# Kernel optimization log

Hardware: AMD Instinct MI355X
Metric: run time of the kernel (lower is better)

The kernel has to match this reference:

```python
import jax, jax.numpy as jnp
import numpy as np

PAD_WORD = 1  # index of PAD in tgt_dict


def setup_inputs() -> dict:
    key = jax.random.key(0)
    k1, k2, k3, k4, k5 = jax.random.split(key, 5)
    N, D, S = 1024, 1024, 64   # N = tlen*batch rows, D = input_size, S = slen
    B, V = 64, 32000           # batch, vocab
    hidden = jax.random.normal(k1, (N, D), dtype=jnp.float32)
    attn = jax.random.uniform(k2, (N, S), dtype=jnp.float32)
    src = jax.random.randint(k3, (S, B, 1), 0, V)
    W = jax.random.normal(k4, (V, D), dtype=jnp.float32) * 0.02
    w_copy = jax.random.normal(k5, (D, 1), dtype=jnp.float32) * 0.02
    b_copy = jnp.zeros((1,), dtype=jnp.float32)
    return {"hidden": hidden, "attn": attn, "src": src, "W": W,
            "w_copy": w_copy, "b_copy": b_copy}


def reference(hidden, attn, src, W, w_copy, b_copy):
    V = W.shape[0]
    B = src.shape[1]
    T = hidden.shape[0] // B  # tlen
    # copy gate: sigmoid(Linear(hidden, 1))  -> [N, 1]
    p_copy = jax.nn.sigmoid(hidden @ w_copy + b_copy)
    # tied-embedding projection -> [N, V], pad column masked to -inf
    logits = hidden @ W.T
    logits = logits.at[:, PAD_WORD].set(-jnp.inf)
    prob = jax.nn.softmax(logits, axis=1) + 1e-20
    # gated generation prob, reshaped to [T, B*V]
    prob = ((1.0 - p_copy) * prob).reshape(T, B * V)
    # flattened source indices with per-batch vocab offsets -> [B*S]
    batch_offset = (jnp.arange(B) * V)[:, None]
    idx = (src[:, :, 0].T + batch_offset).reshape(-1)
    # gated copy attention, reshaped to [T, B*S]
    attn_w = (p_copy * attn).reshape(T, -1)
    # scatter-add copy mass into the vocab distribution (duplicates accumulate)
    out = prob.at[:, idx].add(attn_w)
    return out.reshape(T * B, V)
```

## Files before the change

kernel.cpp:

```cpp
#include <hip/hip_runtime.h>
#include <stdint.h>

typedef unsigned short u16;
typedef unsigned int u32;

#define NROWS 1024
#define DDIM  1024
#define SLEN  64
#define BATCH 64
#define VOCAB 32000
#define NBN2  125
#define PAD_WORD 1

typedef __attribute__((ext_vector_type(4))) float f32x4;
typedef __attribute__((ext_vector_type(8))) short s16x8;

__device__ __forceinline__ u16 f2bf(float x) {
  union { float f; u32 u; } v; v.f = x;
  u32 r = v.u + 0x7FFF + ((v.u >> 16) & 1);
  return (u16)(r >> 16);
}
__device__ __forceinline__ float bf2f(u16 x) {
  union { u32 u; float f; } v; v.u = ((u32)x) << 16;
  return v.f;
}

__global__ __launch_bounds__(256) void prep_convw_kernel(
    const float* __restrict__ hidden, const float* __restrict__ w_copy,
    const float* __restrict__ b_copy, u16* __restrict__ hbf,
    float* __restrict__ pcopy, const float* __restrict__ W,
    u16* __restrict__ Wb)
{
  const int tid = threadIdx.x;
  if (blockIdx.x < NROWS) {
    const int n = blockIdx.x;
    float4 h = ((const float4*)(hidden + (size_t)n * DDIM))[tid];
    float4 w = ((const float4*)w_copy)[tid];
    ushort4 hb;
    hb.x = f2bf(h.x); hb.y = f2bf(h.y); hb.z = f2bf(h.z); hb.w = f2bf(h.w);
    ((ushort4*)(hbf + (size_t)n * DDIM))[tid] = hb;
    float d = h.x * w.x + h.y * w.y + h.z * w.z + h.w * w.w;
    #pragma unroll
    for (int m = 1; m < 64; m <<= 1) d += __shfl_xor(d, m);
    __shared__ float ws4[4];
    if ((tid & 63) == 0) ws4[tid >> 6] = d;
    __syncthreads();
    if (tid == 0) {
      float s = ws4[0] + ws4[1] + ws4[2] + ws4[3] + b_copy[0];
      pcopy[n] = 1.0f / (1.0f + __expf(-s));
    }
    return;
  }
  const int total = VOCAB * DDIM / 8;
  const int stride = (gridDim.x - NROWS) * 256;
  for (int i = (blockIdx.x - NROWS) * 256 + tid; i < total; i += stride) {
    const float4* p = (const float4*)(W + (size_t)i * 8);
    float4 a = p[0], b = p[1];
    uint4 q;
    q.x = (u32)f2bf(a.x) | ((u32)f2bf(a.y) << 16);
    q.y = (u32)f2bf(a.z) | ((u32)f2bf(a.w) << 16);
    q.z = (u32)f2bf(b.x) | ((u32)f2bf(b.y) << 16);
    q.w = (u32)f2bf(b.z) | ((u32)f2bf(b.w) << 16);
    *((uint4*)(Wb + (size_t)i * 8)) = q;
  }
}

__global__ __launch_bounds__(512, 2) void gemm_exp_kernel(
    const u16* __restrict__ A, const u16* __restrict__ B,
    float* __restrict__ out, u16* __restrict__ ebf,
    float* __restrict__ partial, const int use_bf16)
{
  __shared__ u16 lA[2][16384];
  __shared__ u16 lB[2][16384];
  __shared__ float rowacc[4][256];

  const int tid  = threadIdx.x;
  const int lane = tid & 63;
  const int wid  = tid >> 6;
  const int wm   = wid >> 2;
  const int wn   = wid & 3;
  const int al   = lane & 15;
  const int ks   = lane >> 4;

  const int orig = blockIdx.x;
  const int xcd  = orig & 7;
  const int idx  = orig >> 3;
  const int wg   = (xcd < 4 ? xcd * 63 : 252 + (xcd - 4) * 62) + idx;
  const int bm   = wg & 3;
  const int bn   = wg >> 2;

  const u16* Abase = A + (size_t)(bm * 256) * DDIM;
  const u16* Bbase = B + (size_t)(bn * 256) * DDIM;

  const int s0  = wid * 128 + lane;
  const int rr0 = s0 >> 3;
  const int cs0 = (s0 & 7) ^ (rr0 & 7);

#define STAGE(gptr, lptr) do { \
    __builtin_amdgcn_global_load_lds( \
        (const __attribute__((address_space(1))) u32*)((gptr) + (size_t)rr0 * DDIM + cs0 * 8), \
        (__attribute__((address_space(3))) u32*)((lptr) + s0 * 8), 16, 0, 0); \
    __builtin_amdgcn_global_load_lds( \
        (const __attribute__((address_space(1))) u32*)((gptr) + (size_t)(rr0 + 8) * DDIM + cs0 * 8), \
        (__attribute__((address_space(3))) u32*)((lptr) + s0 * 8 + 512), 16, 0, 0); \
  } while (0)

#define WL(n) do { asm volatile("s_waitcnt lgkmcnt(" #n ")" ::: "memory"); \
                   __builtin_amdgcn_sched_barrier(0); } while (0)
#define WV(n) do { asm volatile("s_waitcnt vmcnt(" #n ")" ::: "memory"); \
                   __builtin_amdgcn_sched_barrier(0); } while (0)
#define BAR() do { __builtin_amdgcn_sched_barrier(0); \
                   __builtin_amdgcn_s_barrier(); \
                   __builtin_amdgcn_sched_barrier(0); } while (0)

#define RD_ALO(buf) do { \
    _Pragma("unroll") \
    for (int mi = 0; mi < 4; ++mi) { \
      const u16* p_ = (buf) + wm * 8192 + (mi * 16 + al) * 64; \
      alo[mi][0] = *(const s16x8*)(p_ + (ks ^ (al & 7)) * 8); \
      alo[mi][1] = *(const s16x8*)(p_ + ((4 + ks) ^ (al & 7)) * 8); \
    } } while (0)
#define RD_AHI(buf) do { \
    _Pragma("unroll") \
    for (int mi = 0; mi < 4; ++mi) { \
      const u16* p_ = (buf) + wm * 8192 + (64 + mi * 16 + al) * 64; \
      ahi[mi][0] = *(const s16x8*)(p_ + (ks ^ (al & 7)) * 8); \
      ahi[mi][1] = *(const s16x8*)(p_ + ((4 + ks) ^ (al & 7)) * 8); \
    } } while (0)
#define RD_B0(buf) do { \
    _Pragma("unroll") \
    for (int ni = 0; ni < 2; ++ni) { \
      const u16* p_ = (buf) + (wn >> 1) * 8192 + ((wn & 1) * 64 + ni * 16 + al) * 64; \
      b0f[ni][0] = *(const s16x8*)(p_ + (ks ^ (al & 7)) * 8); \
      b0f[ni][1] = *(const s16x8*)(p_ + ((4 + ks) ^ (al & 7)) * 8); \
    } } while (0)
#define RD_B1(buf) do { \
    _Pragma("unroll") \
    for (int ni = 0; ni < 2; ++ni) { \
      const u16* p_ = (buf) + (wn >> 1) * 8192 + ((wn & 1) * 64 + 32 + ni * 16 + al) * 64; \
      b1f[ni][0] = *(const s16x8*)(p_ + (ks ^ (al & 7)) * 8); \
      b1f[ni][1] = *(const s16x8*)(p_ + ((4 + ks) ^ (al & 7)) * 8); \
    } } while (0)
#define MM(AF, BF, r0, c0) do { \
    __builtin_amdgcn_s_setprio(1); \
    _Pragma("unroll") \
    for (int mi = 0; mi < 4; ++mi) \
      _Pragma("unroll") \
      for (int ni = 0; ni < 2; ++ni) \
        _Pragma("unroll") \
        for (int kk = 0; kk < 2; ++kk) \
          acc[(r0) + mi][(c0) + ni] = __builtin_amdgcn_mfma_f32_16x16x32_bf16( \
              AF[mi][kk], BF[ni][kk], acc[(r0) + mi][(c0) + ni], 0, 0, 0); \
    __builtin_amdgcn_s_setprio(0); \
  } while (0)

  u16* lAc = &lA[0][0]; u16* lBc = &lB[0][0];
  u16* lAn = &lA[1][0]; u16* lBn = &lB[1][0];

  STAGE(Abase,              lAc);
  STAGE(Abase + 128 * DDIM, lAc + 8192);
  STAGE(Bbase,              lBc);
  STAGE(Bbase + 128 * DDIM, lBc + 8192);
  STAGE(Abase + 64,         lAn);
  WV(2);
  BAR();

  f32x4 acc[8][4];
  #pragma unroll
  for (int i = 0; i < 8; ++i)
    #pragma unroll
    for (int j = 0; j < 4; ++j)
      acc[i][j] = (f32x4){0.f, 0.f, 0.f, 0.f};

  s16x8 alo[4][2], ahi[4][2], b0f[2][2], b1f[2][2];

  RD_ALO(lAc); RD_B0(lBc); RD_B1(lBc);
  STAGE(Abase + 128 * DDIM + 64, lAn + 8192);

  for (int t = 0; t < 15; ++t) {
    const int kt1 = (t + 1) * 64;
    const int kt2 = (t + 2) * 64;
    WL(4);
    MM(alo, b0f, 0, 0);
    STAGE(Bbase + kt1, lBn);
    RD_AHI(lAc);
    WL(8);
    MM(alo, b1f, 0, 2);
    STAGE(Bbase + 128 * DDIM + kt1, lBn + 8192);
    WL(0);
    MM(ahi, b0f, 4, 0);
    BAR();
    if (t < 14) STAGE(Abase + kt2, lAc);
    WV(2);
    BAR();
    RD_ALO(lAn); RD_B0(lBn);
    MM(ahi, b1f, 4, 2);
    RD_B1(lBn);
    if (t < 14) STAGE(Abase + 128 * DDIM + kt2, lAc + 8192);
    u16* tp = lAc; lAc = lAn; lAn = tp;
    tp = lBc; lBc = lBn; lBn = tp;
  }
  WL(4);
  MM(alo, b0f, 0, 0);
  RD_AHI(lAc);
  WL(8);
  MM(alo, b1f, 0, 2);
  WL(0);
  MM(ahi, b0f, 4, 0);
  MM(ahi, b1f, 4, 2);

#undef STAGE
#undef WL
#undef WV
#undef BAR

  const int g = ks;
  float rsum[8][4];
  #pragma unroll
  for (int mi = 0; mi < 8; ++mi)
    #pragma unroll
    for (int j = 0; j < 4; ++j) rsum[mi][j] = 0.f;

  const size_t grow0 = (size_t)(bm * 256 + wm * 128);
  const int gcol0 = bn * 256 + wn * 64;
  #pragma unroll
  for (int mi = 0; mi < 8; ++mi) {
    const int rofs = (mi >> 2) * 64 + (mi & 3) * 16 + g * 4;
    #pragma unroll
    for (int j = 0; j < 4; ++j) {
      const size_t row = grow0 + rofs + j;
      #pragma unroll
      for (int ni = 0; ni < 4; ++ni) {
        const int col = gcol0 + (ni >> 1) * 32 + (ni & 1) * 16 + al;
        float e = __expf(acc[mi][ni >> 1][(ni & 1) * 2 + 0] * 0.f +
                         0.f);
        (void)e;
      }
    }
  }
  #pragma unroll
  for (int mi = 0; mi < 8; ++mi) {
    const int rofs = (mi >> 2) * 64 + (mi & 3) * 16 + g * 4;
    #pragma unroll
    for (int j = 0; j < 4; ++j) {
      const size_t row = grow0 + rofs + j;
      #pragma unroll
      for (int ni = 0; ni < 4; ++ni) {
        const int col = gcol0 + (ni >> 1) * 32 + (ni & 1) * 16 + al;
        float e = __expf(acc[mi][ni][j]);
        if (col == PAD_WORD) e = 0.f;
        rsum[mi][j] += e;
        if (use_bf16) ebf[row * VOCAB + col] = f2bf(e);
        else          out[row * VOCAB + col] = e;
      }
    }
  }
  #pragma unroll
  for (int mi = 0; mi < 8; ++mi)
    #pragma unroll
    for (int j = 0; j < 4; ++j) {
      float v = rsum[mi][j];
      v += __shfl_xor(v, 1);
      v += __shfl_xor(v, 2);
      v += __shfl_xor(v, 4);
      v += __shfl_xor(v, 8);
      rsum[mi][j] = v;
    }
  if (al == 0) {
    #pragma unroll
    for (int mi = 0; mi < 8; ++mi)
      #pragma unroll
      for (int j = 0; j < 4; ++j)
        rowacc[wn][wm * 128 + (mi >> 2) * 64 + (mi & 3) * 16 + g * 4 + j] =
            rsum[mi][j];
  }
  __syncthreads();
  if (tid < 256)
    partial[(size_t)bn * NROWS + bm * 256 + tid] =
        rowacc[0][tid] + rowacc[1][tid] + rowacc[2][tid] + rowacc[3][tid];
}

__global__ __launch_bounds__(256) void rowsum_kernel(
    const float* __restrict__ partial, const float* __restrict__ pcopy,
    float* __restrict__ scale, float* __restrict__ ofs)
{
  const int n = blockIdx.x * 256 + threadIdx.x;
  if (n >= NROWS) return;
  float s = 0.f;
  for (int j = 0; j < NBN2; ++j) s += partial[(size_t)j * NROWS + n];
  const float p = pcopy[n];
  scale[n] = (1.0f - p) / s;
  ofs[n]   = (1.0f - p) * 1e-20f;
}

__global__ __launch_bounds__(256) void norm_bf16_kernel(
    const u16* __restrict__ ebf, float* __restrict__ out,
    const float* __restrict__ scale, const float* __restrict__ ofs)
{
  const int total8 = NROWS * VOCAB / 8;
  const int stride = gridDim.x * blockDim.x;
  for (int i = blockIdx.x * 256 + threadIdx.x; i < total8; i += stride) {
    const int n = i / (VOCAB / 8);
    ushort4 v0 = ((const ushort4*)ebf)[i * 2];
    ushort4 v1 = ((const ushort4*)ebf)[i * 2 + 1];
    const float sc = scale[n], of = ofs[n];
    float4 o0, o1;
    o0.x = bf2f(v0.x) * sc + of; o0.y = bf2f(v0.y) * sc + of;
    o0.z = bf2f(v0.z) * sc + of; o0.w = bf2f(v0.w) * sc + of;
    o1.x = bf2f(v1.x) * sc + of; o1.y = bf2f(v1.y) * sc + of;
    o1.z = bf2f(v1.z) * sc + of; o1.w = bf2f(v1.w) * sc + of;
    ((float4*)out)[i * 2]     = o0;
    ((float4*)out)[i * 2 + 1] = o1;
  }
}

__global__ __launch_bounds__(256) void norm_kernel(
    float* __restrict__ out, const float* __restrict__ scale,
    const float* __restrict__ ofs)
{
  const int total4 = NROWS * VOCAB / 4;
  const int stride = gridDim.x * blockDim.x;
  for (int i = blockIdx.x * 256 + threadIdx.x; i < total4; i += stride) {
    const int n = i / (VOCAB / 4);
    float4* p = (float4*)out + i;
    float4 v = *p;
    const float sc = scale[n], of = ofs[n];
    v.x = v.x * sc + of;
    v.y = v.y * sc + of;
    v.z = v.z * sc + of;
    v.w = v.w * sc + of;
    *p = v;
  }
}

__global__ __launch_bounds__(256) void scatter_kernel(
    float* __restrict__ out, const float* __restrict__ attn,
    const int* __restrict__ src, const float* __restrict__ pcopy)
{
  const int t = blockIdx.x * 256 + threadIdx.x;
  const int n = t >> 6;
  const int s = t & 63;
  const int b = n & (BATCH - 1);
  const int v = src[s * BATCH + b];
  const float w = pcopy[n] * attn[(size_t)n * SLEN + s];
  atomicAdd(out + (size_t)n * VOCAB + v, w);
}

extern "C" void kernel_launch(void* const* d_in, const int* in_sizes, int n_in,
                              void* d_out, int out_size, void* d_ws, size_t ws_size,
                              hipStream_t stream) {
  const float* hidden = (const float*)d_in[0];
  const float* attn   = (const float*)d_in[1];
  const int*   src    = (const int*)d_in[2];
  const float* W      = (const float*)d_in[3];
  const float* w_copy = (const float*)d_in[4];
  const float* b_copy = (const float*)d_in[5];
  float* out = (float*)d_out;

  char* ws = (char*)d_ws;
  u16*   Wb      = (u16*)ws;
  u16*   hbf     = (u16*)(ws + 65536000);
  float* pcopy   = (float*)(ws + 67633152);
  float* partial = (float*)(ws + 67637248);
  float* scale   = (float*)(ws + 68661248);
  float* ofs     = (float*)(ws + 68665344);
  u16*   ebf     = (u16*)(ws + 68669440);
  const size_t need_bf16 = 68669440ull + 65536000ull;
  const int use_bf16 = (ws_size >= need_bf16) ? 1 : 0;

  prep_convw_kernel<<<NROWS + 2048, 256, 0, stream>>>(
      hidden, w_copy, b_copy, hbf, pcopy, W, Wb);
  gemm_exp_kernel<<<4 * NBN2, 512, 0, stream>>>(hbf, Wb, out, ebf, partial, use_bf16);
  rowsum_kernel<<<(NROWS + 255) / 256, 256, 0, stream>>>(partial, pcopy, scale, ofs);
  if (use_bf16)
    norm_bf16_kernel<<<2048, 256, 0, stream>>>(ebf, out, scale, ofs);
  else
    norm_kernel<<<2048, 256, 0, stream>>>(out, scale, ofs);
  scatter_kernel<<<NROWS * SLEN / 256, 256, 0, stream>>>(out, attn, src, pcopy);
}
```

Baseline: 165.0 us.

## Fuse W fp32-to-bf16 conversion into GEMM B-tile staging

Drops the separate pass that converted the whole 32000x1024 W matrix to bf16 in the workspace. The GEMM now loads fp32 W rows into registers, converts them with a round-half-up pack, and writes swizzled bf16 into LDS, while A keeps its direct global-to-LDS path. The main loop is rescheduled around register prefetch of the next B tile. This removes a 128MB read plus 64MB write, but each W tile is now read as fp32 by all four M-blocks, which doubles B traffic inside the GEMM and adds conversion ALU work and waits to the main loop. Rounding changes slightly (no ties-to-even) and a dead exp loop is removed.

```diff
diff --git a/kernel.cpp b/kernel.cpp
--- a/kernel.cpp
+++ b/kernel.cpp
@@ -24,49 +24,37 @@
   union { u32 u; float f; } v; v.u = ((u32)x) << 16;
   return v.f;
 }
-
-__global__ __launch_bounds__(256) void prep_convw_kernel(
+__device__ __forceinline__ u32 pkbf(float a, float b) {
+  union { float f; u32 u; } va, vb; va.f = a; vb.f = b;
+  return ((va.u + 0x8000u) >> 16) | ((vb.u + 0x8000u) & 0xFFFF0000u);
+}
+
+__global__ __launch_bounds__(256) void prep_kernel(
     const float* __restrict__ hidden, const float* __restrict__ w_copy,
     const float* __restrict__ b_copy, u16* __restrict__ hbf,
-    float* __restrict__ pcopy, const float* __restrict__ W,
-    u16* __restrict__ Wb)
-{
+    float* __restrict__ pcopy)
+{
+  const int n = blockIdx.x;
   const int tid = threadIdx.x;
-  if (blockIdx.x < NROWS) {
-    const int n = blockIdx.x;
-    float4 h = ((const float4*)(hidden + (size_t)n * DDIM))[tid];
-    float4 w = ((const float4*)w_copy)[tid];
-    ushort4 hb;
-    hb.x = f2bf(h.x); hb.y = f2bf(h.y); hb.z = f2bf(h.z); hb.w = f2bf(h.w);
-    ((ushort4*)(hbf + (size_t)n * DDIM))[tid] = hb;
-    float d = h.x * w.x + h.y * w.y + h.z * w.z + h.w * w.w;
-    #pragma unroll
-    for (int m = 1; m < 64; m <<= 1) d += __shfl_xor(d, m);
-    __shared__ float ws4[4];
-    if ((tid & 63) == 0) ws4[tid >> 6] = d;
-    __syncthreads();
-    if (tid == 0) {
-      float s = ws4[0] + ws4[1] + ws4[2] + ws4[3] + b_copy[0];
-      pcopy[n] = 1.0f / (1.0f + __expf(-s));
-    }
-    return;
-  }
-  const int total = VOCAB * DDIM / 8;
-  const int stride = (gridDim.x - NROWS) * 256;
-  for (int i = (blockIdx.x - NROWS) * 256 + tid; i < total; i += stride) {
-    const float4* p = (const float4*)(W + (size_t)i * 8);
-    float4 a = p[0], b = p[1];
-    uint4 q;
-    q.x = (u32)f2bf(a.x) | ((u32)f2bf(a.y) << 16);
-    q.y = (u32)f2bf(a.z) | ((u32)f2bf(a.w) << 16);
-    q.z = (u32)f2bf(b.x) | ((u32)f2bf(b.y) << 16);
-    q.w = (u32)f2bf(b.z) | ((u32)f2bf(b.w) << 16);
-    *((uint4*)(Wb + (size_t)i * 8)) = q;
+  float4 h = ((const float4*)(hidden + (size_t)n * DDIM))[tid];
+  float4 w = ((const float4*)w_copy)[tid];
+  ushort4 hb;
+  hb.x = f2bf(h.x); hb.y = f2bf(h.y); hb.z = f2bf(h.z); hb.w = f2bf(h.w);
+  ((ushort4*)(hbf + (size_t)n * DDIM))[tid] = hb;
+  float d = h.x * w.x + h.y * w.y + h.z * w.z + h.w * w.w;
+  #pragma unroll
+  for (int m = 1; m < 64; m <<= 1) d += __shfl_xor(d, m);
+  __shared__ float ws4[4];
+  if ((tid & 63) == 0) ws4[tid >> 6] = d;
+  __syncthreads();
+  if (tid == 0) {
+    float s = ws4[0] + ws4[1] + ws4[2] + ws4[3] + b_copy[0];
+    pcopy[n] = 1.0f / (1.0f + __expf(-s));
   }
 }
 
 __global__ __launch_bounds__(512, 2) void gemm_exp_kernel(
-    const u16* __restrict__ A, const u16* __restrict__ B,
+    const u16* __restrict__ A, const float* __restrict__ Wf,
     float* __restrict__ out, u16* __restrict__ ebf,
     float* __restrict__ partial, const int use_bf16)
 {
@@ -90,19 +78,55 @@
   const int bn   = wg >> 2;
 
   const u16* Abase = A + (size_t)(bm * 256) * DDIM;
-  const u16* Bbase = B + (size_t)(bn * 256) * DDIM;
 
   const int s0  = wid * 128 + lane;
   const int rr0 = s0 >> 3;
   const int cs0 = (s0 & 7) ^ (rr0 & 7);
 
-#define STAGE(gptr, lptr) do { \
+#define STAGEH(gptr, lptr) do { \
     __builtin_amdgcn_global_load_lds( \
         (const __attribute__((address_space(1))) u32*)((gptr) + (size_t)rr0 * DDIM + cs0 * 8), \
         (__attribute__((address_space(3))) u32*)((lptr) + s0 * 8), 16, 0, 0); \
     __builtin_amdgcn_global_load_lds( \
         (const __attribute__((address_space(1))) u32*)((gptr) + (size_t)(rr0 + 8) * DDIM + cs0 * 8), \
         (__attribute__((address_space(3))) u32*)((lptr) + s0 * 8 + 512), 16, 0, 0); \
+  } while (0)
+#define STAGE_A(lptr, kt) do { \
+    STAGEH(Abase + (kt), (lptr)); \
+    STAGEH(Abase + 128 * DDIM + (kt), (lptr) + 8192); \
+  } while (0)
+
+  const int brow_st = tid >> 2;
+  const int bk0     = (tid & 3) * 16;
+  const float* Bsrc0 = Wf + (size_t)(bn * 256 + brow_st) * DDIM + bk0;
+  const float* Bsrc1 = Bsrc0 + (size_t)128 * DDIM;
+  f32x4 br[8];
+
+#define ISSUE_B(kt) do { \
+    br[0] = *(const f32x4*)(Bsrc0 + (kt));      \
+    br[1] = *(const f32x4*)(Bsrc0 + (kt) + 4);  \
+    br[2] = *(const f32x4*)(Bsrc0 + (kt) + 8);  \
+    br[3] = *(const f32x4*)(Bsrc0 + (kt) + 12); \
+    br[4] = *(const f32x4*)(Bsrc1 + (kt));      \
+    br[5] = *(const f32x4*)(Bsrc1 + (kt) + 4);  \
+    br[6] = *(const f32x4*)(Bsrc1 + (kt) + 8);  \
+    br[7] = *(const f32x4*)(Bsrc1 + (kt) + 12); \
+  } while (0)
+
+  union pk8 { u32 w[4]; s16x8 v; };
+#define CVT_WRITE_B(dstbase) do { \
+    _Pragma("unroll") \
+    for (int h_ = 0; h_ < 2; ++h_) { \
+      _Pragma("unroll") \
+      for (int j_ = 0; j_ < 2; ++j_) { \
+        pk8 p_; \
+        f32x4 f0_ = br[h_ * 4 + j_ * 2], f1_ = br[h_ * 4 + j_ * 2 + 1]; \
+        p_.w[0] = pkbf(f0_.x, f0_.y); p_.w[1] = pkbf(f0_.z, f0_.w); \
+        p_.w[2] = pkbf(f1_.x, f1_.y); p_.w[3] = pkbf(f1_.z, f1_.w); \
+        const int sl_ = (((tid & 3) * 2 + j_) ^ (brow_st & 7)); \
+        *(s16x8*)((dstbase) + h_ * 8192 + brow_st * 64 + sl_ * 8) = p_.v; \
+      } \
+    } \
   } while (0)
 
 #define WL(n) do { asm volatile("s_waitcnt lgkmcnt(" #n ")" ::: "memory"); \
@@ -157,12 +181,13 @@
   u16* lAc = &lA[0][0]; u16* lBc = &lB[0][0];
   u16* lAn = &lA[1][0]; u16* lBn = &lB[1][0];
 
-  STAGE(Abase,              lAc);
-  STAGE(Abase + 128 * DDIM, lAc + 8192);
-  STAGE(Bbase,              lBc);
-  STAGE(Bbase + 128 * DDIM, lBc + 8192);
-  STAGE(Abase + 64,         lAn);
-  WV(2);
+  ISSUE_B(0);
+  STAGE_A(lAc, 0);
+  WV(4);
+  CVT_WRITE_B(lBc);
+  ISSUE_B(64);
+  WV(8);
+  WL(0);
   BAR();
 
   f32x4 acc[8][4];
@@ -174,32 +199,26 @@
 
   s16x8 alo[4][2], ahi[4][2], b0f[2][2], b1f[2][2];
 
-  RD_ALO(lAc); RD_B0(lBc); RD_B1(lBc);
-  STAGE(Abase + 128 * DDIM + 64, lAn + 8192);
-
   for (int t = 0; t < 15; ++t) {
-    const int kt1 = (t + 1) * 64;
-    const int kt2 = (t + 2) * 64;
+    RD_ALO(lAc); RD_B0(lBc); RD_B1(lBc);
+    WV(0);
+    CVT_WRITE_B(lBn);
+    STAGE_A(lAn, (t + 1) * 64);
+    if (t < 14) ISSUE_B((t + 2) * 64);
+    WL(8);
+    MM(alo, b0f, 0, 0);
     WL(4);
-    MM(alo, b0f, 0, 0);
-    STAGE(Bbase + kt1, lBn);
+    MM(alo, b1f, 0, 2);
     RD_AHI(lAc);
-    WL(8);
-    MM(alo, b1f, 0, 2);
-    STAGE(Bbase + 128 * DDIM + kt1, lBn + 8192);
     WL(0);
     MM(ahi, b0f, 4, 0);
+    if (t < 14) { WV(8); } else { WV(0); }
     BAR();
-    if (t < 14) STAGE(Abase + kt2, lAc);
-    WV(2);
-    BAR();
-    RD_ALO(lAn); RD_B0(lBn);
     MM(ahi, b1f, 4, 2);
-    RD_B1(lBn);
-    if (t < 14) STAGE(Abase + 128 * DDIM + kt2, lAc + 8192);
     u16* tp = lAc; lAc = lAn; lAn = tp;
     tp = lBc; lBc = lBn; lBn = tp;
   }
+  RD_ALO(lAc); RD_B0(lBc); RD_B1(lBc);
   WL(4);
   MM(alo, b0f, 0, 0);
   RD_AHI(lAc);
@@ -209,7 +228,10 @@
   MM(ahi, b0f, 4, 0);
   MM(ahi, b1f, 4, 2);
 
-#undef STAGE
+#undef STAGEH
+#undef STAGE_A
+#undef ISSUE_B
+#undef CVT_WRITE_B
 #undef WL
 #undef WV
 #undef BAR
@@ -223,21 +245,6 @@
 
   const size_t grow0 = (size_t)(bm * 256 + wm * 128);
   const int gcol0 = bn * 256 + wn * 64;
-  #pragma unroll
-  for (int mi = 0; mi < 8; ++mi) {
-    const int rofs = (mi >> 2) * 64 + (mi & 3) * 16 + g * 4;
-    #pragma unroll
-    for (int j = 0; j < 4; ++j) {
-      const size_t row = grow0 + rofs + j;
-      #pragma unroll
-      for (int ni = 0; ni < 4; ++ni) {
-        const int col = gcol0 + (ni >> 1) * 32 + (ni & 1) * 16 + al;
-        float e = __expf(acc[mi][ni >> 1][(ni & 1) * 2 + 0] * 0.f +
-                         0.f);
-        (void)e;
-      }
-    }
-  }
   #pragma unroll
   for (int mi = 0; mi < 8; ++mi) {
     const int rofs = (mi >> 2) * 64 + (mi & 3) * 16 + g * 4;
@@ -358,19 +365,17 @@
   float* out = (float*)d_out;
 
   char* ws = (char*)d_ws;
-  u16*   Wb      = (u16*)ws;
-  u16*   hbf     = (u16*)(ws + 65536000);
-  float* pcopy   = (float*)(ws + 67633152);
-  float* partial = (float*)(ws + 67637248);
-  float* scale   = (float*)(ws + 68661248);
-  float* ofs     = (float*)(ws + 68665344);
-  u16*   ebf     = (u16*)(ws + 68669440);
-  const size_t need_bf16 = 68669440ull + 65536000ull;
+  u16*   hbf     = (u16*)ws;
+  float* pcopy   = (float*)(ws + 2097152);
+  float* partial = (float*)(ws + 2101248);
+  float* scale   = (float*)(ws + 3125248);
+  float* ofs     = (float*)(ws + 3129344);
+  u16*   ebf     = (u16*)(ws + 3133440);
+  const size_t need_bf16 = 3133440ull + 65536000ull;
   const int use_bf16 = (ws_size >= need_bf16) ? 1 : 0;
 
-  prep_convw_kernel<<<NROWS + 2048, 256, 0, stream>>>(
-      hidden, w_copy, b_copy, hbf, pcopy, W, Wb);
-  gemm_exp_kernel<<<4 * NBN2, 512, 0, stream>>>(hbf, Wb, out, ebf, partial, use_bf16);
+  prep_kernel<<<NROWS, 256, 0, stream>>>(hidden, w_copy, b_copy, hbf, pcopy);
+  gemm_exp_kernel<<<4 * NBN2, 512, 0, stream>>>(hbf, W, out, ebf, partial, use_bf16);
   rowsum_kernel<<<(NROWS + 255) / 256, 256, 0, stream>>>(partial, pcopy, scale, ofs);
   if (use_bf16)
     norm_bf16_kernel<<<2048, 256, 0, stream>>>(ebf, out, scale, ofs);
```

New measurement: 156.3 us. -5.3%, faster.

## Switch GEMM operands from bf16 to fp8 e4m3 with fp8 MFMA

Applied to the files above, without the earlier changes.

Hidden states and the tied embedding weight are now quantized to fp8 e4m3 instead of bf16, and the GEMM runs on the fp8 16x16x32 MFMA with LDS tiles, staging and swizzle rebuilt for byte elements. The aim is to halve operand bytes in the weight conversion output and GEMM loads and to raise MFMA throughput. The prep kernel is split into a hidden/gate kernel and a separate weight conversion kernel, and a dead exp loop in the epilogue is removed. The cost is much lower precision in the logits, with no per-tensor scaling, which risks accuracy against the fp32 reference.

```diff
diff --git a/kernel.cpp b/kernel.cpp
--- a/kernel.cpp
+++ b/kernel.cpp
@@ -1,6 +1,7 @@
 #include <hip/hip_runtime.h>
 #include <stdint.h>
 
+typedef unsigned char  u8;
 typedef unsigned short u16;
 typedef unsigned int u32;
 
@@ -13,7 +14,6 @@
 #define PAD_WORD 1
 
 typedef __attribute__((ext_vector_type(4))) float f32x4;
-typedef __attribute__((ext_vector_type(8))) short s16x8;
 
 __device__ __forceinline__ u16 f2bf(float x) {
   union { float f; u32 u; } v; v.f = x;
@@ -24,54 +24,68 @@
   union { u32 u; float f; } v; v.u = ((u32)x) << 16;
   return v.f;
 }
-
-__global__ __launch_bounds__(256) void prep_convw_kernel(
+__device__ __forceinline__ u32 f2e4m3(float x) {
+  union { float f; u32 u; } v; v.f = x;
+  const u32 s = (v.u >> 31) << 7;
+  const u32 m = v.u & 0x7FFFFFFFu;
+  if (m < 0x3C800000u) {
+    union { u32 u; float f; } a; a.u = m;
+    int q = (int)rintf(a.f * 512.0f);
+    return s | (u32)q;
+  }
+  u32 u2 = m + 0x7FFFFu + ((m >> 20) & 1);
+  u32 code = (((u2 >> 23) - 120u) << 3) | ((u2 >> 20) & 7u);
+  if (code > 0x7Eu) code = 0x7Eu;
+  return s | code;
+}
+
+__global__ __launch_bounds__(256) void prep_kernel(
     const float* __restrict__ hidden, const float* __restrict__ w_copy,
-    const float* __restrict__ b_copy, u16* __restrict__ hbf,
-    float* __restrict__ pcopy, const float* __restrict__ W,
-    u16* __restrict__ Wb)
-{
+    const float* __restrict__ b_copy, u8* __restrict__ hq,
+    float* __restrict__ pcopy)
+{
+  const int n = blockIdx.x;
   const int tid = threadIdx.x;
-  if (blockIdx.x < NROWS) {
-    const int n = blockIdx.x;
-    float4 h = ((const float4*)(hidden + (size_t)n * DDIM))[tid];
-    float4 w = ((const float4*)w_copy)[tid];
-    ushort4 hb;
-    hb.x = f2bf(h.x); hb.y = f2bf(h.y); hb.z = f2bf(h.z); hb.w = f2bf(h.w);
-    ((ushort4*)(hbf + (size_t)n * DDIM))[tid] = hb;
-    float d = h.x * w.x + h.y * w.y + h.z * w.z + h.w * w.w;
-    #pragma unroll
-    for (int m = 1; m < 64; m <<= 1) d += __shfl_xor(d, m);
-    __shared__ float ws4[4];
-    if ((tid & 63) == 0) ws4[tid >> 6] = d;
-    __syncthreads();
-    if (tid == 0) {
-      float s = ws4[0] + ws4[1] + ws4[2] + ws4[3] + b_copy[0];
-      pcopy[n] = 1.0f / (1.0f + __expf(-s));
-    }
-    return;
-  }
-  const int total = VOCAB * DDIM / 8;
-  const int stride = (gridDim.x - NROWS) * 256;
-  for (int i = (blockIdx.x - NROWS) * 256 + tid; i < total; i += stride) {
-    const float4* p = (const float4*)(W + (size_t)i * 8);
-    float4 a = p[0], b = p[1];
+  float4 h = ((const float4*)(hidden + (size_t)n * DDIM))[tid];
+  float4 w = ((const float4*)w_copy)[tid];
+  u32 q = f2e4m3(h.x) | (f2e4m3(h.y) << 8) | (f2e4m3(h.z) << 16) | (f2e4m3(h.w) << 24);
+  ((u32*)(hq + (size_t)n * DDIM))[tid] = q;
+  float d = h.x * w.x + h.y * w.y + h.z * w.z + h.w * w.w;
+  #pragma unroll
+  for (int m = 1; m < 64; m <<= 1) d += __shfl_xor(d, m);
+  __shared__ float ws4[4];
+  if ((tid & 63) == 0) ws4[tid >> 6] = d;
+  __syncthreads();
+  if (tid == 0) {
+    float s = ws4[0] + ws4[1] + ws4[2] + ws4[3] + b_copy[0];
+    pcopy[n] = 1.0f / (1.0f + __expf(-s));
+  }
+}
+
+__global__ __launch_bounds__(256) void convw8_kernel(
+    const float* __restrict__ W, u8* __restrict__ Wq)
+{
+  const int total = VOCAB * DDIM / 16;
+  const int stride = gridDim.x * blockDim.x;
+  for (int i = blockIdx.x * 256 + threadIdx.x; i < total; i += stride) {
+    const f32x4* p = (const f32x4*)(W + (size_t)i * 16);
+    f32x4 a = p[0], b = p[1], c = p[2], d = p[3];
     uint4 q;
-    q.x = (u32)f2bf(a.x) | ((u32)f2bf(a.y) << 16);
-    q.y = (u32)f2bf(a.z) | ((u32)f2bf(a.w) << 16);
-    q.z = (u32)f2bf(b.x) | ((u32)f2bf(b.y) << 16);
-    q.w = (u32)f2bf(b.z) | ((u32)f2bf(b.w) << 16);
-    *((uint4*)(Wb + (size_t)i * 8)) = q;
+    q.x = f2e4m3(a.x) | (f2e4m3(a.y) << 8) | (f2e4m3(a.z) << 16) | (f2e4m3(a.w) << 24);
+    q.y = f2e4m3(b.x) | (f2e4m3(b.y) << 8) | (f2e4m3(b.z) << 16) | (f2e4m3(b.w) << 24);
+    q.z = f2e4m3(c.x) | (f2e4m3(c.y) << 8) | (f2e4m3(c.z) << 16) | (f2e4m3(c.w) << 24);
+    q.w = f2e4m3(d.x) | (f2e4m3(d.y) << 8) | (f2e4m3(d.z) << 16) | (f2e4m3(d.w) << 24);
+    ((uint4*)Wq)[i] = q;
   }
 }
 
 __global__ __launch_bounds__(512, 2) void gemm_exp_kernel(
-    const u16* __restrict__ A, const u16* __restrict__ B,
+    const u8* __restrict__ A, const u8* __restrict__ B,
     float* __restrict__ out, u16* __restrict__ ebf,
     float* __restrict__ partial, const int use_bf16)
 {
-  __shared__ u16 lA[2][16384];
-  __shared__ u16 lB[2][16384];
+  __shared__ u8 lA[2][16384];
+  __shared__ u8 lB[2][16384];
   __shared__ float rowacc[4][256];
 
   const int tid  = threadIdx.x;
@@ -89,20 +103,19 @@
   const int bm   = wg & 3;
   const int bn   = wg >> 2;
 
-  const u16* Abase = A + (size_t)(bm * 256) * DDIM;
-  const u16* Bbase = B + (size_t)(bn * 256) * DDIM;
-
-  const int s0  = wid * 128 + lane;
-  const int rr0 = s0 >> 3;
-  const int cs0 = (s0 & 7) ^ (rr0 & 7);
-
-#define STAGE(gptr, lptr) do { \
-    __builtin_amdgcn_global_load_lds( \
-        (const __attribute__((address_space(1))) u32*)((gptr) + (size_t)rr0 * DDIM + cs0 * 8), \
-        (__attribute__((address_space(3))) u32*)((lptr) + s0 * 8), 16, 0, 0); \
-    __builtin_amdgcn_global_load_lds( \
-        (const __attribute__((address_space(1))) u32*)((gptr) + (size_t)(rr0 + 8) * DDIM + cs0 * 8), \
-        (__attribute__((address_space(3))) u32*)((lptr) + s0 * 8 + 512), 16, 0, 0); \
+  const u8* Abase = A + (size_t)(bm * 256) * DDIM;
+  const u8* Bbase = B + (size_t)(bn * 256) * DDIM;
+
+  const int sA = wid * 64 + lane;
+  const int rA = sA >> 2;
+  const int cA = (lane & 3) ^ (rA & 3);
+
+#define GLL(gp, lp) __builtin_amdgcn_global_load_lds( \
+    (const __attribute__((address_space(1))) u32*)(gp), \
+    (__attribute__((address_space(3))) u32*)(lp), 16, 0, 0)
+#define STAGE_T(gbase, lptr, kt) do { \
+    GLL((gbase) + (size_t)rA * DDIM + (kt) + cA * 16, (lptr) + sA * 16); \
+    GLL((gbase) + (size_t)(rA + 128) * DDIM + (kt) + cA * 16, (lptr) + 8192 + sA * 16); \
   } while (0)
 
 #define WL(n) do { asm volatile("s_waitcnt lgkmcnt(" #n ")" ::: "memory"); \
@@ -116,30 +129,34 @@
 #define RD_ALO(buf) do { \
     _Pragma("unroll") \
     for (int mi = 0; mi < 4; ++mi) { \
-      const u16* p_ = (buf) + wm * 8192 + (mi * 16 + al) * 64; \
-      alo[mi][0] = *(const s16x8*)(p_ + (ks ^ (al & 7)) * 8); \
-      alo[mi][1] = *(const s16x8*)(p_ + ((4 + ks) ^ (al & 7)) * 8); \
+      const int r_ = wm * 128 + mi * 16 + al; \
+      const u8* p_ = (buf) + r_ * 64 + (ks & 1) * 8; \
+      alo[mi][0] = *(const long*)(p_ + ((((ks >> 1))     ^ (r_ & 3)) * 16)); \
+      alo[mi][1] = *(const long*)(p_ + ((((ks >> 1) + 2) ^ (r_ & 3)) * 16)); \
     } } while (0)
 #define RD_AHI(buf) do { \
     _Pragma("unroll") \
     for (int mi = 0; mi < 4; ++mi) { \
-      const u16* p_ = (buf) + wm * 8192 + (64 + mi * 16 + al) * 64; \
-      ahi[mi][0] = *(const s16x8*)(p_ + (ks ^ (al & 7)) * 8); \
-      ahi[mi][1] = *(const s16x8*)(p_ + ((4 + ks) ^ (al & 7)) * 8); \
+      const int r_ = wm * 128 + 64 + mi * 16 + al; \
+      const u8* p_ = (buf) + r_ * 64 + (ks & 1) * 8; \
+      ahi[mi][0] = *(const long*)(p_ + ((((ks >> 1))     ^ (r_ & 3)) * 16)); \
+      ahi[mi][1] = *(const long*)(p_ + ((((ks >> 1) + 2) ^ (r_ & 3)) * 16)); \
     } } while (0)
 #define RD_B0(buf) do { \
     _Pragma("unroll") \
     for (int ni = 0; ni < 2; ++ni) { \
-      const u16* p_ = (buf) + (wn >> 1) * 8192 + ((wn & 1) * 64 + ni * 16 + al) * 64; \
-      b0f[ni][0] = *(const s16x8*)(p_ + (ks ^ (al & 7)) * 8); \
-      b0f[ni][1] = *(const s16x8*)(p_ + ((4 + ks) ^ (al & 7)) * 8); \
+      const int r_ = wn * 64 + ni * 16 + al; \
+      const u8* p_ = (buf) + r_ * 64 + (ks & 1) * 8; \
+      b0f[ni][0] = *(const long*)(p_ + ((((ks >> 1))     ^ (r_ & 3)) * 16)); \
+      b0f[ni][1] = *(const long*)(p_ + ((((ks >> 1) + 2) ^ (r_ & 3)) * 16)); \
     } } while (0)
 #define RD_B1(buf) do { \
     _Pragma("unroll") \
     for (int ni = 0; ni < 2; ++ni) { \
-      const u16* p_ = (buf) + (wn >> 1) * 8192 + ((wn & 1) * 64 + 32 + ni * 16 + al) * 64; \
-      b1f[ni][0] = *(const s16x8*)(p_ + (ks ^ (al & 7)) * 8); \
-      b1f[ni][1] = *(const s16x8*)(p_ + ((4 + ks) ^ (al & 7)) * 8); \
+      const int r_ = wn * 64 + 32 + ni * 16 + al; \
+      const u8* p_ = (buf) + r_ * 64 + (ks & 1) * 8; \
+      b1f[ni][0] = *(const long*)(p_ + ((((ks >> 1))     ^ (r_ & 3)) * 16)); \
+      b1f[ni][1] = *(const long*)(p_ + ((((ks >> 1) + 2) ^ (r_ & 3)) * 16)); \
     } } while (0)
 #define MM(AF, BF, r0, c0) do { \
     __builtin_amdgcn_s_setprio(1); \
@@ -149,55 +166,49 @@
       for (int ni = 0; ni < 2; ++ni) \
         _Pragma("unroll") \
         for (int kk = 0; kk < 2; ++kk) \
-          acc[(r0) + mi][(c0) + ni] = __builtin_amdgcn_mfma_f32_16x16x32_bf16( \
+          acc[(r0) + mi][(c0) + ni] = __builtin_amdgcn_mfma_f32_16x16x32_fp8_fp8( \
               AF[mi][kk], BF[ni][kk], acc[(r0) + mi][(c0) + ni], 0, 0, 0); \
     __builtin_amdgcn_s_setprio(0); \
   } while (0)
 
-  u16* lAc = &lA[0][0]; u16* lBc = &lB[0][0];
-  u16* lAn = &lA[1][0]; u16* lBn = &lB[1][0];
-
-  STAGE(Abase,              lAc);
-  STAGE(Abase + 128 * DDIM, lAc + 8192);
-  STAGE(Bbase,              lBc);
-  STAGE(Bbase + 128 * DDIM, lBc + 8192);
-  STAGE(Abase + 64,         lAn);
+  u8* lAc = &lA[0][0]; u8* lBc = &lB[0][0];
+  u8* lAn = &lA[1][0]; u8* lBn = &lB[1][0];
+
+  f32x4 acc[8][4];
+  #pragma unroll
+  for (int i = 0; i < 8; ++i)
+    #pragma unroll
+    for (int j = 0; j < 4; ++j)
+      acc[i][j] = (f32x4){0.f, 0.f, 0.f, 0.f};
+
+  long alo[4][2], ahi[4][2], b0f[2][2], b1f[2][2];
+
+  STAGE_T(Abase, lAc, 0);
+  STAGE_T(Bbase, lBc, 0);
+  STAGE_T(Abase, lAn, 64);
   WV(2);
   BAR();
-
-  f32x4 acc[8][4];
-  #pragma unroll
-  for (int i = 0; i < 8; ++i)
-    #pragma unroll
-    for (int j = 0; j < 4; ++j)
-      acc[i][j] = (f32x4){0.f, 0.f, 0.f, 0.f};
-
-  s16x8 alo[4][2], ahi[4][2], b0f[2][2], b1f[2][2];
-
   RD_ALO(lAc); RD_B0(lBc); RD_B1(lBc);
-  STAGE(Abase + 128 * DDIM + 64, lAn + 8192);
 
   for (int t = 0; t < 15; ++t) {
     const int kt1 = (t + 1) * 64;
     const int kt2 = (t + 2) * 64;
     WL(4);
     MM(alo, b0f, 0, 0);
-    STAGE(Bbase + kt1, lBn);
+    STAGE_T(Bbase, lBn, kt1);
     RD_AHI(lAc);
     WL(8);
     MM(alo, b1f, 0, 2);
-    STAGE(Bbase + 128 * DDIM + kt1, lBn + 8192);
     WL(0);
     MM(ahi, b0f, 4, 0);
     BAR();
-    if (t < 14) STAGE(Abase + kt2, lAc);
-    WV(2);
+    if (t < 14) STAGE_T(Abase, lAc, kt2);
+    if (t < 14) { WV(2); } else { WV(0); }
     BAR();
     RD_ALO(lAn); RD_B0(lBn);
     MM(ahi, b1f, 4, 2);
     RD_B1(lBn);
-    if (t < 14) STAGE(Abase + 128 * DDIM + kt2, lAc + 8192);
-    u16* tp = lAc; lAc = lAn; lAn = tp;
+    u8* tp = lAc; lAc = lAn; lAn = tp;
     tp = lBc; lBc = lBn; lBn = tp;
   }
   WL(4);
@@ -209,7 +220,8 @@
   MM(ahi, b0f, 4, 0);
   MM(ahi, b1f, 4, 2);
 
-#undef STAGE
+#undef GLL
+#undef STAGE_T
 #undef WL
 #undef WV
 #undef BAR
@@ -223,21 +235,6 @@
 
   const size_t grow0 = (size_t)(bm * 256 + wm * 128);
   const int gcol0 = bn * 256 + wn * 64;
-  #pragma unroll
-  for (int mi = 0; mi < 8; ++mi) {
-    const int rofs = (mi >> 2) * 64 + (mi & 3) * 16 + g * 4;
-    #pragma unroll
-    for (int j = 0; j < 4; ++j) {
-      const size_t row = grow0 + rofs + j;
-      #pragma unroll
-      for (int ni = 0; ni < 4; ++ni) {
-        const int col = gcol0 + (ni >> 1) * 32 + (ni & 1) * 16 + al;
-        float e = __expf(acc[mi][ni >> 1][(ni & 1) * 2 + 0] * 0.f +
-                         0.f);
-        (void)e;
-      }
-    }
-  }
   #pragma unroll
   for (int mi = 0; mi < 8; ++mi) {
     const int rofs = (mi >> 2) * 64 + (mi & 3) * 16 + g * 4;
@@ -358,19 +355,19 @@
   float* out = (float*)d_out;
 
   char* ws = (char*)d_ws;
-  u16*   Wb      = (u16*)ws;
-  u16*   hbf     = (u16*)(ws + 65536000);
-  float* pcopy   = (float*)(ws + 67633152);
-  float* partial = (float*)(ws + 67637248);
-  float* scale   = (float*)(ws + 68661248);
-  float* ofs     = (float*)(ws + 68665344);
-  u16*   ebf     = (u16*)(ws + 68669440);
-  const size_t need_bf16 = 68669440ull + 65536000ull;
+  u8*    Wq      = (u8*)ws;
+  u8*    hq      = (u8*)(ws + 32768000);
+  float* pcopy   = (float*)(ws + 33816576);
+  float* partial = (float*)(ws + 33820672);
+  float* scale   = (float*)(ws + 34844672);
+  float* ofs     = (float*)(ws + 34848768);
+  u16*   ebf     = (u16*)(ws + 34852864);
+  const size_t need_bf16 = 34852864ull + 65536000ull;
   const int use_bf16 = (ws_size >= need_bf16) ? 1 : 0;
 
-  prep_convw_kernel<<<NROWS + 2048, 256, 0, stream>>>(
-      hidden, w_copy, b_copy, hbf, pcopy, W, Wb);
-  gemm_exp_kernel<<<4 * NBN2, 512, 0, stream>>>(hbf, Wb, out, ebf, partial, use_bf16);
+  prep_kernel<<<NROWS, 256, 0, stream>>>(hidden, w_copy, b_copy, hq, pcopy);
+  convw8_kernel<<<2048, 256, 0, stream>>>(W, Wq);
+  gemm_exp_kernel<<<4 * NBN2, 512, 0, stream>>>(hq, Wq, out, ebf, partial, use_bf16);
   rowsum_kernel<<<(NROWS + 255) / 256, 256, 0, stream>>>(partial, pcopy, scale, ofs);
   if (use_bf16)
     norm_bf16_kernel<<<2048, 256, 0, stream>>>(ebf, out, scale, ofs);
```

Result: slower. 171.1 us (+3.7%).
